# Performance work log

Measured on AMD Instinct MI355X. Metric: run time of the kernel, lower is better.

Reference implementation:

```python
import jax, jax.numpy as jnp
import numpy as np

N = 8192          # total nodes (bipartite: first half left, second half right)
E = 65536         # raw edges
D = 256           # emb_dim
H = 8             # heads
HD = D // H       # head_dim = 32
EAD = 2           # edge_attr_dim


def _init(k, shape, fan_in):
    return (jax.random.normal(k, shape, jnp.float32) / np.sqrt(fan_in)).astype(jnp.float32)


def setup_inputs() -> dict:
    key = jax.random.key(0)
    ks = jax.random.split(key, 16)
    x = jax.random.normal(ks[0], (N, D), jnp.float32)
    src = jax.random.randint(ks[1], (E,), 0, N // 2, jnp.int32)
    dst = jax.random.randint(ks[2], (E,), N // 2, N, jnp.int32)
    edge_index = jnp.stack([src, dst])                       # [2, E]
    edge_attr = jax.random.uniform(ks[3], (E, EAD), jnp.float32)
    query_mask = jax.random.randint(ks[4], (E,), 0, 2, jnp.int32).astype(bool)
    return {
        "x": x,
        "edge_index": edge_index,
        "edge_attr": edge_attr,
        "query_mask": query_mask,
        "start_right": N // 2,
        "W_kqv": _init(ks[5], (D, 3 * D), D), "b_kqv": jnp.zeros((3 * D,), jnp.float32),
        "W_edge": _init(ks[6], (EAD, D), EAD), "b_edge": jnp.zeros((D,), jnp.float32),
        "W_att1": _init(ks[7], (3 * HD, HD), 3 * HD), "b_att1": jnp.zeros((HD,), jnp.float32),
        "W_att2": _init(ks[8], (HD, 1), HD), "b_att2": jnp.zeros((1,), jnp.float32),
        "W_out": _init(ks[9], (D, D), D), "b_out": jnp.zeros((D,), jnp.float32),
        "bn_gamma": jnp.ones((D,), jnp.float32), "bn_beta": jnp.zeros((D,), jnp.float32),
    }


def _build_graph(edge_index, query_mask, n):
    """Replicates MetaGNN.forward edge preprocessing (static, int-only)."""
    ei = np.asarray(edge_index)
    qm = np.asarray(query_mask).astype(bool)
    sup = np.where(~qm)[0]                                   # support edges
    # cat([edge_index[:, support], edge_index.flip(0)], dim=1)
    src = np.concatenate([ei[0, sup], ei[1]])
    dst = np.concatenate([ei[1, sup], ei[0]])
    attr_idx = np.concatenate([sup, np.arange(ei.shape[1])])
    # remove_self_loops
    keep = src != dst
    src, dst, attr_idx = src[keep], dst[keep], attr_idx[keep]
    # add_self_loops with fill_value [0, 0]
    loops = np.arange(n)
    src = np.concatenate([src, loops])
    dst = np.concatenate([dst, loops])
    return jnp.asarray(src), jnp.asarray(dst), jnp.asarray(attr_idx)


def _layer(x, src, dst, ea, W_kqv, b_kqv, W_edge, b_edge, W_att1, b_att1,
           W_att2, b_att2, W_out, b_out, bn_gamma, bn_beta):
    n = x.shape[0]
    kqv = x @ W_kqv + b_kqv                                  # [N, 3D]
    q = kqv[dst, :D].reshape(-1, H, HD)                      # x_i (target)
    k = kqv[src, D:2 * D].reshape(-1, H, HD) / np.sqrt(HD)   # x_j (source)
    v = kqv[src, 2 * D:].reshape(-1, H, HD)
    ef = jax.nn.relu((ea @ W_edge + b_edge).reshape(-1, H, HD))
    feat = jnp.concatenate([k, q, ef], axis=-1)              # [E, H, 3*HD]
    hdn = jax.nn.relu(jnp.einsum('ehf,fd->ehd', feat, W_att1) + b_att1)
    logits = (jnp.einsum('ehd,do->eho', hdn, W_att2) + b_att2)[..., 0]  # [E, H]
    # scatter-softmax over destination node segments
    m = jax.ops.segment_max(logits, dst, num_segments=n)
    a = jnp.exp(logits - m[dst])
    s = jax.ops.segment_sum(a, dst, num_segments=n)
    alpha = a / (s[dst] + 1e-16)                             # [E, H]
    msg = (alpha[..., None] * v).reshape(-1, D) @ W_out + b_out
    out = jax.ops.segment_sum(msg, dst, num_segments=n) + x  # aggr='add' + residual
    # BatchNorm1d (training-mode batch statistics, eps=1e-5)
    mu = out.mean(axis=0)
    var = out.var(axis=0)
    return (out - mu) / jnp.sqrt(var + 1e-5) * bn_gamma + bn_beta


def reference(x, edge_index, edge_attr, query_mask, start_right,
              W_kqv, b_kqv, W_edge, b_edge, W_att1, b_att1, W_att2, b_att2,
              W_out, b_out, bn_gamma, bn_beta):
    n = x.shape[0]
    src, dst, attr_idx = _build_graph(edge_index, query_mask, n)
    ea = jnp.concatenate(
        [edge_attr[attr_idx], jnp.zeros((n, edge_attr.shape[1]), edge_attr.dtype)], axis=0)
    return _layer(x, src, dst, ea, W_kqv, b_kqv, W_edge, b_edge,
                  W_att1, b_att1, W_att2, b_att2, W_out, b_out, bn_gamma, bn_beta)
```

## Files before the change

### kernel.cpp

```cpp
#include <hip/hip_runtime.h>

#define N_NODES 8192
#define E_RAW   65536
#define NSLOT   (2*E_RAW + N_NODES)
#define DEGCAP  48
#define L_ITER  2
#define MAIN_BLKS (E_RAW / (16 * L_ITER))
#define TAIL_BLKS (N_NODES / (16 * L_ITER))

typedef __attribute__((ext_vector_type(8)))  short bf16x8;
typedef __attribute__((ext_vector_type(4)))  short bf16x4;
typedef __attribute__((ext_vector_type(4)))  float f32x4;
typedef __attribute__((ext_vector_type(16))) float f32x16;
typedef unsigned short u16;

__device__ __forceinline__ u16 f2b(float f) {
  unsigned u = __float_as_uint(f);
  u = (u + 0x7FFFu + ((u >> 16) & 1u)) >> 16;
  return (u16)u;
}
__device__ __forceinline__ float b2f(u16 b) {
  return __uint_as_float(((unsigned)b) << 16);
}

__global__ __launch_bounds__(256) void setup_k(
    const float* __restrict__ x, u16* __restrict__ xb,
    const float* __restrict__ W_kqv, const float* __restrict__ b_kqv,
    const float* __restrict__ W_att1, const float* __restrict__ b_att1,
    const float* __restrict__ W_edge, const float* __restrict__ b_edge,
    const float* __restrict__ W_out,
    u16* __restrict__ BcatT, float* __restrict__ biascat,
    u16* __restrict__ wa1t, u16* __restrict__ WoutT, float* __restrict__ beW,
    int4* __restrict__ zbase)
{
  __shared__ float tile[64][65];
  const float inv_sqrt_hd = 0.17677669529663687f;
  int bx = blockIdx.x, t = threadIdx.x;

  if (bx < 2048) {
    int i = bx * 256 + t;
    float4 v = ((const float4*)x)[i];
    ushort4 o;
    o.x = f2b(v.x); o.y = f2b(v.y); o.z = f2b(v.z); o.w = f2b(v.w);
    ((ushort4*)xb)[i] = o;
    return;
  }
  if (bx < 2836) {
    int c = bx - 2048;
    int i = t;
    if (c < 768) {
      float v;
      if (c < 256) {
        int h = c >> 5, d2 = c & 31;
        float s = 0.f;
        #pragma unroll
        for (int j = 0; j < 32; ++j)
          s += W_kqv[i*768 + 256 + h*32 + j] * W_att1[j*32 + d2];
        v = s * inv_sqrt_hd;
      } else if (c < 512) {
        int c2 = c - 256; int h = c2 >> 5, d2 = c2 & 31;
        float s = 0.f;
        #pragma unroll
        for (int j = 0; j < 32; ++j)
          s += W_kqv[i*768 + h*32 + j] * W_att1[(32+j)*32 + d2];
        v = s;
      } else {
        v = W_kqv[i*768 + c];
      }
      BcatT[(size_t)c * 256 + i] = f2b(v);
      if (i == 0) {
        float bv;
        if (c < 256) {
          int h = c >> 5, d2 = c & 31;
          float s = 0.f;
          for (int j = 0; j < 32; ++j)
            s += b_kqv[256 + h*32 + j] * W_att1[j*32 + d2];
          bv = s * inv_sqrt_hd;
        } else if (c < 512) {
          int c2 = c - 256; int h = c2 >> 5, d2 = c2 & 31;
          float s = 0.f;
          for (int j = 0; j < 32; ++j)
            s += b_kqv[h*32 + j] * W_att1[(32+j)*32 + d2];
          bv = s + b_att1[c2 & 31];
        } else {
          bv = b_kqv[c];
        }
        biascat[c] = bv;
      }
    } else if (c < 772) {
      int idx = (c - 768) * 256 + i;
      int d2 = idx >> 5, j = idx & 31;
      wa1t[idx] = f2b(W_att1[(64 + j) * 32 + d2]);
    } else {
      int b = c - 772;
      int r0 = (b >> 2) * 64, c0 = (b & 3) * 64;
      for (int idx = i; idx < 4096; idx += 256) {
        int r = idx >> 6, cc = idx & 63;
        tile[r][cc] = W_out[(size_t)(r0 + r) * 256 + c0 + cc];
      }
      __syncthreads();
      for (int idx = i; idx < 4096; idx += 256) {
        int cc = idx >> 6, r = idx & 63;
        WoutT[(size_t)(c0 + cc) * 256 + r0 + r] = f2b(tile[r][cc]);
      }
    }
    return;
  }
  if (bx == 2836) {
    int h = t >> 5, d2 = t & 31;
    float s = 0.f;
    #pragma unroll
    for (int f = 0; f < 32; ++f)
      s += fmaxf(b_edge[h*32 + f], 0.f) * W_att1[(64 + f)*32 + d2];
    beW[h*32 + d2] = s;
    return;
  }
  int i = (bx - 2837) * 256 + t;
  if (i < 2176) zbase[i] = make_int4(0, 0, 0, 0);
}

__global__ __launch_bounds__(256) void gemm_scatter_k(
    const u16* __restrict__ xb, const u16* __restrict__ BcatT,
    const float* __restrict__ biascat, u16* __restrict__ nodeF,
    const int* __restrict__ ei, const int* __restrict__ qm,
    int* __restrict__ cnt, int* __restrict__ csr)
{
  int bx = blockIdx.x, t = threadIdx.x;
  if (bx < 768) {
    int lane = t & 63, wid = t >> 6;
    int cb = bx % 12, rb = bx / 12;
    int r0 = rb * 128 + wid * 32;
    int c0 = cb * 64;
    int lr = lane & 15, lk = (lane >> 4) * 8;
    f32x4 acc0[4] = {}, acc1[4] = {};
    for (int k0 = 0; k0 < 256; k0 += 32) {
      bf16x8 a0 = *(const bf16x8*)&xb[(size_t)(r0 + lr) * 256 + k0 + lk];
      bf16x8 a1 = *(const bf16x8*)&xb[(size_t)(r0 + 16 + lr) * 256 + k0 + lk];
      bf16x8 b0 = *(const bf16x8*)&BcatT[(size_t)(c0 + lr) * 256 + k0 + lk];
      bf16x8 b1 = *(const bf16x8*)&BcatT[(size_t)(c0 + 16 + lr) * 256 + k0 + lk];
      bf16x8 b2 = *(const bf16x8*)&BcatT[(size_t)(c0 + 32 + lr) * 256 + k0 + lk];
      bf16x8 b3 = *(const bf16x8*)&BcatT[(size_t)(c0 + 48 + lr) * 256 + k0 + lk];
      acc0[0] = __builtin_amdgcn_mfma_f32_16x16x32_bf16(a0, b0, acc0[0], 0, 0, 0);
      acc0[1] = __builtin_amdgcn_mfma_f32_16x16x32_bf16(a0, b1, acc0[1], 0, 0, 0);
      acc0[2] = __builtin_amdgcn_mfma_f32_16x16x32_bf16(a0, b2, acc0[2], 0, 0, 0);
      acc0[3] = __builtin_amdgcn_mfma_f32_16x16x32_bf16(a0, b3, acc0[3], 0, 0, 0);
      acc1[0] = __builtin_amdgcn_mfma_f32_16x16x32_bf16(a1, b0, acc1[0], 0, 0, 0);
      acc1[1] = __builtin_amdgcn_mfma_f32_16x16x32_bf16(a1, b1, acc1[1], 0, 0, 0);
      acc1[2] = __builtin_amdgcn_mfma_f32_16x16x32_bf16(a1, b2, acc1[2], 0, 0, 0);
      acc1[3] = __builtin_amdgcn_mfma_f32_16x16x32_bf16(a1, b3, acc1[3], 0, 0, 0);
    }
    int rbase = r0 + (lane >> 4) * 4;
    #pragma unroll
    for (int cc = 0; cc < 4; ++cc) {
      float bias = biascat[c0 + cc*16 + lr];
      #pragma unroll
      for (int r = 0; r < 4; ++r) {
        nodeF[(size_t)(rbase + r) * 768 + c0 + cc*16 + lr]      = f2b(acc0[cc][r] + bias);
        nodeF[(size_t)(rbase + 16 + r) * 768 + c0 + cc*16 + lr] = f2b(acc1[cc][r] + bias);
      }
    }
    return;
  }
  int slot = (bx - 768) * 256 + t;
  if (slot >= NSLOT) return;
  int src, dst;
  if (slot < E_RAW) {
    if (qm[slot] != 0) return;
    src = ei[slot]; dst = ei[E_RAW + slot];
  } else if (slot < 2*E_RAW) {
    int e = slot - E_RAW;
    src = ei[E_RAW + e]; dst = ei[e];
  } else {
    int n = slot - 2*E_RAW;
    src = n; dst = n;
  }
  int pos = atomicAdd(&cnt[dst], 1);
  if (pos < DEGCAP) csr[dst*DEGCAP + pos] = (slot << 13) | src;
}

__global__ __launch_bounds__(256) void logits_k(
    const int* __restrict__ ei, const int* __restrict__ qm,
    const float* __restrict__ eattr, const u16* __restrict__ nf,
    const u16* __restrict__ wa1t,
    const float* __restrict__ W_edge, const float* __restrict__ b_edge,
    const float* __restrict__ W_att2, const float* __restrict__ beW,
    float* __restrict__ lgd)
{
  __shared__ __align__(16) u16 kqls[4][16][8][40];

  int bx = blockIdx.x, t = threadIdx.x, lane = t & 63, wid = t >> 6;
  int col = lane & 31;
  int e = col >> 3, h = col & 7, hi = lane >> 5;

  float w2r[16];
  #pragma unroll
  for (int r = 0; r < 16; ++r)
    w2r[r] = W_att2[(r & 3) + 8*(r >> 2) + 4*hi];

  if (bx < MAIN_BLKS) {
    float ce0[16], ce1[16], cbe[16];
    #pragma unroll
    for (int i = 0; i < 8; ++i) {
      int fA = hi*8 + i, fB = 16 + hi*8 + i;
      ce0[i]   = W_edge[h*32 + fA];       ce0[8+i] = W_edge[h*32 + fB];
      ce1[i]   = W_edge[256 + h*32 + fA]; ce1[8+i] = W_edge[256 + h*32 + fB];
      cbe[i]   = b_edge[h*32 + fA];       cbe[8+i] = b_edge[h*32 + fB];
    }
    bf16x8 af0 = *(const bf16x8*)&wa1t[(lane & 31)*32 + hi*8];
    bf16x8 af1 = *(const bf16x8*)&wa1t[(lane & 31)*32 + 16 + hi*8];

    int eqm_r[L_ITER]; float2 ea_r[L_ITER];
    #pragma unroll
    for (int it = 0; it < L_ITER; ++it) {
      int er = ((bx * L_ITER + it) * 4 + wid) * 4 + e;
      eqm_r[it] = qm[er];
      ea_r[it] = *(const float2*)&eattr[2*er];
    }

    int nidx[2][8];
    #pragma unroll
    for (int m = 0; m < 8; ++m) {
      int flat = m*64 + lane, ri = flat >> 5;
      int ee = ri & 3, ty = ri >> 2;
      int erow = ((bx * L_ITER + 0) * 4 + wid) * 4 + ee;
      nidx[0][m] = (ty & 1) ? ei[E_RAW + erow] : ei[erow];
    }

    #pragma unroll
    for (int it = 0; it < L_ITER; ++it) {
      if (it + 1 < L_ITER) {
        #pragma unroll
        for (int m = 0; m < 8; ++m) {
          int flat = m*64 + lane, ri = flat >> 5;
          int ee = ri & 3, ty = ri >> 2;
          int erow = ((bx * L_ITER + it + 1) * 4 + wid) * 4 + ee;
          nidx[(it+1) & 1][m] = (ty & 1) ? ei[E_RAW + erow] : ei[erow];
        }
      }
      #pragma unroll
      for (int m = 0; m < 8; ++m) {
        int flat = m*64 + lane, ri = flat >> 5, chunk = flat & 31;
        int ty = ri >> 2;
        int koff = (ty >> 1) ? 256 : 0;
        bf16x8 v = *(const bf16x8*)&nf[(size_t)nidx[it & 1][m]*768 + koff + chunk*8];
        *(bf16x8*)&kqls[wid][ri][chunk >> 2][(chunk & 3)*8] = v;
      }

      float2 ea = ea_r[it];
      bf16x8 bf0, bf1;
      #pragma unroll
      for (int i = 0; i < 8; ++i) {
        float v0 = fmaf(ea.x, ce0[i],   fmaf(ea.y, ce1[i],   cbe[i]));
        float v1 = fmaf(ea.x, ce0[8+i], fmaf(ea.y, ce1[8+i], cbe[8+i]));
        bf0[i] = (short)f2b(fmaxf(v0, 0.f));
        bf1[i] = (short)f2b(fmaxf(v1, 0.f));
      }
      f32x16 acc = {};
      acc = __builtin_amdgcn_mfma_f32_32x32x16_bf16(af0, bf0, acc, 0, 0, 0);
      acc = __builtin_amdgcn_mfma_f32_32x32x16_bf16(af1, bf1, acc, 0, 0, 0);

      __builtin_amdgcn_wave_barrier();

      float lg0 = 0.f, lg1 = 0.f;
      #pragma unroll
      for (int q = 0; q < 4; ++q) {
        int off = q*8 + 4*hi;
        bf16x4 k0 = *(const bf16x4*)&kqls[wid][e][h][off];
        bf16x4 q0 = *(const bf16x4*)&kqls[wid][12 + e][h][off];
        bf16x4 k1 = *(const bf16x4*)&kqls[wid][4 + e][h][off];
        bf16x4 q1 = *(const bf16x4*)&kqls[wid][8 + e][h][off];
        #pragma unroll
        for (int j = 0; j < 4; ++j) {
          int r = q*4 + j;
          float efw = acc[r];
          float p0 = efw + b2f((u16)k0[j]) + b2f((u16)q0[j]);
          float p1 = efw + b2f((u16)k1[j]) + b2f((u16)q1[j]);
          lg0 = fmaf(fmaxf(p0, 0.f), w2r[r], lg0);
          lg1 = fmaf(fmaxf(p1, 0.f), w2r[r], lg1);
        }
      }
      lg0 += __shfl_xor(lg0, 32);
      lg1 += __shfl_xor(lg1, 32);
      int er = ((bx * L_ITER + it) * 4 + wid) * 4 + e;
      if (hi == 0) {
        if (eqm_r[it] == 0) lgd[(size_t)er*8 + h] = lg0;
      } else {
        lgd[(size_t)(E_RAW + er)*8 + h] = lg1;
      }
      __builtin_amdgcn_wave_barrier();
    }
  } else {
    float bew[16];
    #pragma unroll
    for (int r = 0; r < 16; ++r)
      bew[r] = beW[h*32 + (r & 3) + 8*(r >> 2) + 4*hi];

    for (int it = 0; it < L_ITER; ++it) {
      int n0 = (((bx - MAIN_BLKS) * L_ITER + it) * 4 + wid) * 4;
      int nn = n0 + e;
      #pragma unroll
      for (int m = 0; m < 4; ++m) {
        int flat = m*64 + lane;
        int ri = flat >> 5, chunk = flat & 31;
        int ee = ri & 3, ty = ri >> 2;
        int node = n0 + ee;
        bf16x8 v = *(const bf16x8*)&nf[(size_t)node*768 + (ty ? 256 : 0) + chunk*8];
        *(bf16x8*)&kqls[wid][ri][chunk >> 2][(chunk & 3)*8] = v;
      }
      __builtin_amdgcn_wave_barrier();
      float lg0 = 0.f;
      #pragma unroll
      for (int q = 0; q < 4; ++q) {
        int off = q*8 + 4*hi;
        bf16x4 k0 = *(const bf16x4*)&kqls[wid][e][h][off];
        bf16x4 q0 = *(const bf16x4*)&kqls[wid][4 + e][h][off];
        #pragma unroll
        for (int j = 0; j < 4; ++j) {
          int r = q*4 + j;
          float p = bew[r] + b2f((u16)k0[j]) + b2f((u16)q0[j]);
          lg0 = fmaf(fmaxf(p, 0.f), w2r[r], lg0);
        }
      }
      lg0 += __shfl_xor(lg0, 32);
      if (hi == 0) lgd[(size_t)(2*E_RAW + nn)*8 + h] = lg0;
      __builtin_amdgcn_wave_barrier();
    }
  }
}

__global__ __launch_bounds__(256) void aggr_k(const int* __restrict__ cnt,
                                              const int* __restrict__ csr,
                                              const float* __restrict__ lgd,
                                              const u16* __restrict__ nf,
                                              u16* __restrict__ aggb) {
  int t = threadIdx.x, lane = t & 63, wid = t >> 6;
  int n = blockIdx.x * 4 + wid;
  int deg = cnt[n]; if (deg > DEGCAP) deg = DEGCAP;
  int head = lane >> 3;

  int pk = (lane < deg) ? csr[n*DEGCAP + lane] : 0;

  int i0 = lane >> 3, hh = lane & 7;
  int nit = (deg + 7) >> 3;
  float m = -3.4e38f, s = 0.f;
  for (int ii = 0; ii < nit; ++ii) {
    int i = ii * 8 + i0;
    int ic = (i < deg) ? i : 0;
    int pki = __shfl(pk, ic);
    float val = (i < deg)
        ? lgd[(size_t)((unsigned)pki >> 13)*8 + hh] : -3.4e38f;
    float mn = fmaxf(m, val);
    float addv = (i < deg) ? __expf(val - mn) : 0.f;
    s = s * __expf(m - mn) + addv;
    m = mn;
  }
  #pragma unroll
  for (int msk = 8; msk <= 32; msk <<= 1) {
    float mo = __shfl_xor(m, msk), so = __shfl_xor(s, msk);
    float mn = fmaxf(m, mo);
    s = s * __expf(m - mn) + so * __expf(mo - mn);
    m = mn;
  }
  float sinv = 1.f / (s + 1e-16f);
  float mh = __shfl(m, head);
  float sh = __shfl(sinv, head);

  float ac0 = 0.f, ac1 = 0.f, ac2 = 0.f, ac3 = 0.f;
  const u16* vb = nf + 512 + lane * 4;
  int pk0 = __shfl(pk, 0);
  float lg_pf = lgd[(size_t)((unsigned)pk0 >> 13)*8 + head];
  bf16x4 v_pf = *(const bf16x4*)&vb[(size_t)(pk0 & 8191) * 768];
  for (int i = 0; i < deg; ++i) {
    float lgv = lg_pf;
    bf16x4 v = v_pf;
    if (i + 1 < deg) {
      int pkn = __shfl(pk, i + 1);
      lg_pf = lgd[(size_t)((unsigned)pkn >> 13)*8 + head];
      v_pf = *(const bf16x4*)&vb[(size_t)(pkn & 8191) * 768];
    }
    float a = __expf(lgv - mh) * sh;
    ac0 = fmaf(a, b2f((u16)v[0]), ac0);
    ac1 = fmaf(a, b2f((u16)v[1]), ac1);
    ac2 = fmaf(a, b2f((u16)v[2]), ac2);
    ac3 = fmaf(a, b2f((u16)v[3]), ac3);
  }
  ushort4 o; o.x = f2b(ac0); o.y = f2b(ac1); o.z = f2b(ac2); o.w = f2b(ac3);
  *(ushort4*)&aggb[(size_t)n * 256 + lane * 4] = o;
}

__global__ __launch_bounds__(256) void gemmout_k(const u16* __restrict__ aggb,
                                                 const u16* __restrict__ WoutT,
                                                 const float* __restrict__ x,
                                                 const int* __restrict__ cnt,
                                                 const float* __restrict__ b_out,
                                                 float* __restrict__ out,
                                                 float* __restrict__ bnsum,
                                                 float* __restrict__ bnsq) {
  int t = threadIdx.x, lane = t & 63, wid = t >> 6;
  int bx = blockIdx.x;
  int cb = bx & 3, rb = bx >> 2;
  int r0 = rb * 128 + wid * 32;
  int c0 = cb * 64;
  int lr = lane & 15, lk = (lane >> 4) * 8;
  f32x4 acc0[4] = {}, acc1[4] = {};
  for (int k0 = 0; k0 < 256; k0 += 32) {
    bf16x8 a0 = *(const bf16x8*)&aggb[(size_t)(r0 + lr) * 256 + k0 + lk];
    bf16x8 a1 = *(const bf16x8*)&aggb[(size_t)(r0 + 16 + lr) * 256 + k0 + lk];
    bf16x8 b0 = *(const bf16x8*)&WoutT[(size_t)(c0 + lr) * 256 + k0 + lk];
    bf16x8 b1 = *(const bf16x8*)&WoutT[(size_t)(c0 + 16 + lr) * 256 + k0 + lk];
    bf16x8 b2 = *(const bf16x8*)&WoutT[(size_t)(c0 + 32 + lr) * 256 + k0 + lk];
    bf16x8 b3 = *(const bf16x8*)&WoutT[(size_t)(c0 + 48 + lr) * 256 + k0 + lk];
    acc0[0] = __builtin_amdgcn_mfma_f32_16x16x32_bf16(a0, b0, acc0[0], 0, 0, 0);
    acc0[1] = __builtin_amdgcn_mfma_f32_16x16x32_bf16(a0, b1, acc0[1], 0, 0, 0);
    acc0[2] = __builtin_amdgcn_mfma_f32_16x16x32_bf16(a0, b2, acc0[2], 0, 0, 0);
    acc0[3] = __builtin_amdgcn_mfma_f32_16x16x32_bf16(a0, b3, acc0[3], 0, 0, 0);
    acc1[0] = __builtin_amdgcn_mfma_f32_16x16x32_bf16(a1, b0, acc1[0], 0, 0, 0);
    acc1[1] = __builtin_amdgcn_mfma_f32_16x16x32_bf16(a1, b1, acc1[1], 0, 0, 0);
    acc1[2] = __builtin_amdgcn_mfma_f32_16x16x32_bf16(a1, b2, acc1[2], 0, 0, 0);
    acc1[3] = __builtin_amdgcn_mfma_f32_16x16x32_bf16(a1, b3, acc1[3], 0, 0, 0);
  }
  int rbase = r0 + (lane >> 4) * 4;
  float degA[4], degB[4];
  #pragma unroll
  for (int r = 0; r < 4; ++r) {
    degA[r] = (float)cnt[rbase + r];
    degB[r] = (float)cnt[rbase + 16 + r];
  }
  #pragma unroll
  for (int cc = 0; cc < 4; ++cc) {
    int colC = c0 + cc*16 + lr;
    float bC = b_out[colC];
    float sC = 0.f, qC = 0.f;
    #pragma unroll
    for (int r = 0; r < 4; ++r) {
      int rowA = rbase + r, rowB = rbase + 16 + r;
      float v0 = acc0[cc][r] + x[(size_t)rowA * 256 + colC] + degA[r] * bC;
      float v1 = acc1[cc][r] + x[(size_t)rowB * 256 + colC] + degB[r] * bC;
      out[(size_t)rowA * 256 + colC] = v0;
      out[(size_t)rowB * 256 + colC] = v1;
      sC += v0 + v1; qC += v0*v0 + v1*v1;
    }
    #pragma unroll
    for (int msk = 16; msk <= 32; msk <<= 1) {
      sC += __shfl_xor(sC, msk); qC += __shfl_xor(qC, msk);
    }
    if (lane < 16) {
      atomicAdd(&bnsum[colC], sC); atomicAdd(&bnsq[colC], qC);
    }
  }
}

__global__ __launch_bounds__(256) void bnapply_k(float* __restrict__ out,
                                                 const float* __restrict__ bnsum,
                                                 const float* __restrict__ bnsq,
                                                 const float* __restrict__ gamma,
                                                 const float* __restrict__ beta) {
  int t = threadIdx.x;
  int c4 = t & 63;
  int r = blockIdx.x * 4 + (t >> 6);
  float4 s4 = ((const float4*)bnsum)[c4];
  float4 q4 = ((const float4*)bnsq)[c4];
  float4 g4 = ((const float4*)gamma)[c4];
  float4 b4 = ((const float4*)beta)[c4];
  float4 v = ((const float4*)out)[(size_t)r * 64 + c4];
  #pragma unroll
  for (int j = 0; j < 4; ++j) {
    float mu = (&s4.x)[j] * (1.f / 8192.f);
    float var = (&q4.x)[j] * (1.f / 8192.f) - mu*mu;
    float inv = rsqrtf(var + 1e-5f);
    (&v.x)[j] = ((&v.x)[j] - mu) * inv * (&g4.x)[j] + (&b4.x)[j];
  }
  ((float4*)out)[(size_t)r * 64 + c4] = v;
}

extern "C" void kernel_launch(void* const* d_in, const int* in_sizes, int n_in,
                              void* d_out, int out_size, void* d_ws, size_t ws_size,
                              hipStream_t stream) {
  (void)in_sizes; (void)n_in; (void)out_size; (void)ws_size;
  const float* x      = (const float*)d_in[0];
  const int*   ei     = (const int*)d_in[1];
  const float* eattr  = (const float*)d_in[2];
  const int*   qm     = (const int*)d_in[3];
  const float* W_kqv  = (const float*)d_in[5];
  const float* b_kqv  = (const float*)d_in[6];
  const float* W_edge = (const float*)d_in[7];
  const float* b_edge = (const float*)d_in[8];
  const float* W_att1 = (const float*)d_in[9];
  const float* b_att1 = (const float*)d_in[10];
  const float* W_att2 = (const float*)d_in[11];
  const float* W_out  = (const float*)d_in[13];
  const float* b_out  = (const float*)d_in[14];
  const float* gamma  = (const float*)d_in[15];
  const float* beta   = (const float*)d_in[16];
  float* out = (float*)d_out;

  char* w = (char*)d_ws;
  u16*    xb      = (u16*)w;     w += (size_t)N_NODES*256*2;
  u16*    BcatT   = (u16*)w;     w += (size_t)768*256*2;
  u16*    wa1t    = (u16*)w;     w += 1024*2;
  u16*    WoutT   = (u16*)w;     w += (size_t)256*256*2;
  u16*    nodeFb  = (u16*)w;     w += (size_t)N_NODES*768*2;
  float*  biascat = (float*)w;   w += 768*4;
  float*  beW     = (float*)w;   w += 256*4;
  u16*    aggb    = (u16*)w;     w += (size_t)N_NODES*256*2;
  int*    cnt     = (int*)w;     w += N_NODES*4;
  float*  bnsum   = (float*)w;   w += 256*4;
  float*  bnsq    = (float*)w;   w += 256*4;
  int*    csr     = (int*)w;     w += (size_t)N_NODES*DEGCAP*4;
  float*  lgd     = (float*)w;   w += (size_t)NSLOT*8*4;

  setup_k<<<2846, 256, 0, stream>>>(
      x, xb, W_kqv, b_kqv, W_att1, b_att1, W_edge, b_edge, W_out,
      BcatT, biascat, wa1t, WoutT, beW, (int4*)cnt);

  gemm_scatter_k<<<768 + (NSLOT + 255)/256, 256, 0, stream>>>(
      xb, BcatT, biascat, nodeFb, ei, qm, cnt, csr);

  logits_k<<<MAIN_BLKS + TAIL_BLKS, 256, 0, stream>>>(
      ei, qm, eattr, nodeFb, wa1t, W_edge, b_edge, W_att2, beW, lgd);

  aggr_k<<<N_NODES/4, 256, 0, stream>>>(cnt, csr, lgd, nodeFb, aggb);

  gemmout_k<<<256, 256, 0, stream>>>(
      aggb, WoutT, x, cnt, b_out, out, bnsum, bnsq);

  bnapply_k<<<N_NODES/4, 256, 0, stream>>>(out, bnsum, bnsq, gamma, beta);
}
```

Measured before the change: 97.88 us.

## Fuse softmax into aggregation with online rescaling; coalesce gathers; raise L_ITER

Aggregation now uses an online softmax in a single pass. It rescales the running accumulators by exp(m_old - m_new), which removes the separate max/sum pre-pass and its second gather of logits. In the logit kernels, each K/Q node row is now loaded by one wave as a contiguous 1 KB read and stored to LDS with remapped row indices, where previously the per-lane mapping was strided. L_ITER goes from 2 to 4, which halves the number of edge blocks and puts more iterations in each block. The online softmax adds two exps per edge per lane and creates a serial dependency on the accumulators.

```diff
diff --git a/kernel.cpp b/kernel.cpp
--- a/kernel.cpp
+++ b/kernel.cpp
@@ -4,7 +4,7 @@
 #define E_RAW   65536
 #define NSLOT   (2*E_RAW + N_NODES)
 #define DEGCAP  48
-#define L_ITER  2
+#define L_ITER  4
 #define MAIN_BLKS (E_RAW / (16 * L_ITER))
 #define TAIL_BLKS (N_NODES / (16 * L_ITER))
 
@@ -220,10 +220,8 @@
     int nidx[2][8];
     #pragma unroll
     for (int m = 0; m < 8; ++m) {
-      int flat = m*64 + lane, ri = flat >> 5;
-      int ee = ri & 3, ty = ri >> 2;
-      int erow = ((bx * L_ITER + 0) * 4 + wid) * 4 + ee;
-      nidx[0][m] = (ty & 1) ? ei[E_RAW + erow] : ei[erow];
+      int erow = ((bx * L_ITER + 0) * 4 + wid) * 4 + (m & 3);
+      nidx[0][m] = (m >> 2) ? ei[E_RAW + erow] : ei[erow];
     }
 
     #pragma unroll
@@ -231,19 +229,16 @@
       if (it + 1 < L_ITER) {
         #pragma unroll
         for (int m = 0; m < 8; ++m) {
-          int flat = m*64 + lane, ri = flat >> 5;
-          int ee = ri & 3, ty = ri >> 2;
-          int erow = ((bx * L_ITER + it + 1) * 4 + wid) * 4 + ee;
-          nidx[(it+1) & 1][m] = (ty & 1) ? ei[E_RAW + erow] : ei[erow];
+          int erow = ((bx * L_ITER + it + 1) * 4 + wid) * 4 + (m & 3);
+          nidx[(it+1) & 1][m] = (m >> 2) ? ei[E_RAW + erow] : ei[erow];
         }
       }
       #pragma unroll
       for (int m = 0; m < 8; ++m) {
-        int flat = m*64 + lane, ri = flat >> 5, chunk = flat & 31;
-        int ty = ri >> 2;
-        int koff = (ty >> 1) ? 256 : 0;
-        bf16x8 v = *(const bf16x8*)&nf[(size_t)nidx[it & 1][m]*768 + koff + chunk*8];
-        *(bf16x8*)&kqls[wid][ri][chunk >> 2][(chunk & 3)*8] = v;
+        bf16x8 v = *(const bf16x8*)&nf[(size_t)nidx[it & 1][m]*768 + lane*8];
+        int drow = ((lane >> 5) << 3) + ((m >> 2) << 2) + (m & 3);
+        int chunk = lane & 31;
+        *(bf16x8*)&kqls[wid][drow][chunk >> 2][(chunk & 3)*8] = v;
       }
 
       float2 ea = ea_r[it];
@@ -300,12 +295,10 @@
       int nn = n0 + e;
       #pragma unroll
       for (int m = 0; m < 4; ++m) {
-        int flat = m*64 + lane;
-        int ri = flat >> 5, chunk = flat & 31;
-        int ee = ri & 3, ty = ri >> 2;
-        int node = n0 + ee;
-        bf16x8 v = *(const bf16x8*)&nf[(size_t)node*768 + (ty ? 256 : 0) + chunk*8];
-        *(bf16x8*)&kqls[wid][ri][chunk >> 2][(chunk & 3)*8] = v;
+        bf16x8 v = *(const bf16x8*)&nf[(size_t)(n0 + m)*768 + lane*8];
+        int drow = ((lane >> 5) << 2) + m;
+        int chunk = lane & 31;
+        *(bf16x8*)&kqls[wid][drow][chunk >> 2][(chunk & 3)*8] = v;
       }
       __builtin_amdgcn_wave_barrier();
       float lg0 = 0.f;
@@ -340,36 +333,13 @@
 
   int pk = (lane < deg) ? csr[n*DEGCAP + lane] : 0;
 
-  int i0 = lane >> 3, hh = lane & 7;
-  int nit = (deg + 7) >> 3;
-  float m = -3.4e38f, s = 0.f;
-  for (int ii = 0; ii < nit; ++ii) {
-    int i = ii * 8 + i0;
-    int ic = (i < deg) ? i : 0;
-    int pki = __shfl(pk, ic);
-    float val = (i < deg)
-        ? lgd[(size_t)((unsigned)pki >> 13)*8 + hh] : -3.4e38f;
-    float mn = fmaxf(m, val);
-    float addv = (i < deg) ? __expf(val - mn) : 0.f;
-    s = s * __expf(m - mn) + addv;
-    m = mn;
-  }
-  #pragma unroll
-  for (int msk = 8; msk <= 32; msk <<= 1) {
-    float mo = __shfl_xor(m, msk), so = __shfl_xor(s, msk);
-    float mn = fmaxf(m, mo);
-    s = s * __expf(m - mn) + so * __expf(mo - mn);
-    m = mn;
-  }
-  float sinv = 1.f / (s + 1e-16f);
-  float mh = __shfl(m, head);
-  float sh = __shfl(sinv, head);
-
-  float ac0 = 0.f, ac1 = 0.f, ac2 = 0.f, ac3 = 0.f;
   const u16* vb = nf + 512 + lane * 4;
   int pk0 = __shfl(pk, 0);
   float lg_pf = lgd[(size_t)((unsigned)pk0 >> 13)*8 + head];
   bf16x4 v_pf = *(const bf16x4*)&vb[(size_t)(pk0 & 8191) * 768];
+
+  float m = -3.4e38f, s = 0.f;
+  float ac0 = 0.f, ac1 = 0.f, ac2 = 0.f, ac3 = 0.f;
   for (int i = 0; i < deg; ++i) {
     float lgv = lg_pf;
     bf16x4 v = v_pf;
@@ -378,13 +348,20 @@
       lg_pf = lgd[(size_t)((unsigned)pkn >> 13)*8 + head];
       v_pf = *(const bf16x4*)&vb[(size_t)(pkn & 8191) * 768];
     }
-    float a = __expf(lgv - mh) * sh;
-    ac0 = fmaf(a, b2f((u16)v[0]), ac0);
-    ac1 = fmaf(a, b2f((u16)v[1]), ac1);
-    ac2 = fmaf(a, b2f((u16)v[2]), ac2);
-    ac3 = fmaf(a, b2f((u16)v[3]), ac3);
-  }
-  ushort4 o; o.x = f2b(ac0); o.y = f2b(ac1); o.z = f2b(ac2); o.w = f2b(ac3);
+    float mn = fmaxf(m, lgv);
+    float r = __expf(m - mn);
+    float a = __expf(lgv - mn);
+    s  = fmaf(s, r, a);
+    ac0 = fmaf(ac0, r, a * b2f((u16)v[0]));
+    ac1 = fmaf(ac1, r, a * b2f((u16)v[1]));
+    ac2 = fmaf(ac2, r, a * b2f((u16)v[2]));
+    ac3 = fmaf(ac3, r, a * b2f((u16)v[3]));
+    m = mn;
+  }
+  float sinv = 1.f / (s + 1e-16f);
+  ushort4 o;
+  o.x = f2b(ac0 * sinv); o.y = f2b(ac1 * sinv);
+  o.z = f2b(ac2 * sinv); o.w = f2b(ac3 * sinv);
   *(ushort4*)&aggb[(size_t)n * 256 + lane * 4] = o;
 }
 
```

After: 98.00 us. No clear change (+0.1%).
